# Kernel tuning notes

Hardware: AMD Instinct MI355X
Metric: run time of the kernel (lower is better)

Reference implementation:

```python
import jax, jax.numpy as jnp
import numpy as np

G = 64  # voxel grid extent per axis; grid_ind entries are in [0, G)


def setup_inputs() -> dict:
    key = jax.random.key(0)
    k1, k2 = jax.random.split(key)
    N = 4_000_000
    points = jax.random.normal(k1, (N, 7), dtype=jnp.float32)
    grid_ind = jax.random.randint(k2, (N, 3), 0, G, dtype=jnp.int64)
    return {"points": points, "grid_ind": grid_ind}


def reference(points, grid_ind):
    # torch.unique(grid_ind, dim=0, return_inverse=True) sorts rows
    # lexicographically; for nonnegative coords that equals sorting the
    # linearized index, so we dedup the linear id instead of rows.
    N = points.shape[0]
    gi = grid_ind.astype(jnp.int32)
    lin = (gi[:, 0] * G + gi[:, 1]) * G + gi[:, 2]  # [N]
    # fixed-size unique for jit compatibility: at most N unique voxels,
    # padded with fill_value=-1 at the tail.
    unq, unq_inv = jnp.unique(lin, return_inverse=True, size=N, fill_value=-1)
    # scatter_mean over point->voxel mapping
    sums = jax.ops.segment_sum(points, unq_inv, num_segments=N)          # [N, 7]
    cnt = jax.ops.segment_sum(jnp.ones((N,), points.dtype), unq_inv,
                              num_segments=N)                            # [N]
    mean = sums / jnp.maximum(cnt, 1.0)[:, None]
    # reconstruct the [n_unique_padded, 3] voxel coordinates (pad rows = -1)
    valid = unq >= 0
    u = jnp.maximum(unq, 0)
    unq3 = jnp.stack([u // (G * G), (u // G) % G, u % G], axis=-1)
    unq3 = jnp.where(valid[:, None], unq3, -1).astype(grid_ind.dtype)
    return mean, unq3
```

## Files before the change

### kernel.cpp

```cpp
#include <hip/hip_runtime.h>

#define NVOX 262144
#define NB   256
#define VPB  1024
#define PPB  2048
#define SCT  512
#define NBLK 256

__global__ void dv_fill(const unsigned* __restrict__ nuP,
                        float* __restrict__ out, int n) {
    int nu = (int)*nuP;
    size_t meanChunks = (size_t)n * 7 / 4;
    size_t coordChunks = (size_t)n * 3 / 4;
    size_t total = meanChunks + coordChunks;
    size_t i = (size_t)blockIdx.x * blockDim.x + threadIdx.x;
    if (i >= total) return;
    float* mean = out;
    float* coords = out + (size_t)n * 7;
    if (i < meanChunks) {
        size_t base = i * 4, lim = (size_t)nu * 7;
        if (base >= lim) {
            *(float4*)(mean + base) = make_float4(0.f, 0.f, 0.f, 0.f);
        } else if (base + 4 > lim) {
            for (size_t k = lim; k < base + 4; ++k) mean[k] = 0.f;
        }
    } else {
        size_t base = (i - meanChunks) * 4, lim = (size_t)nu * 3;
        if (base >= lim) {
            *(float4*)(coords + base) = make_float4(-1.f, -1.f, -1.f, -1.f);
        } else if (base + 4 > lim) {
            for (size_t k = lim; k < base + 4; ++k) coords[k] = -1.f;
        }
    }
}

__device__ __forceinline__ unsigned bf16rne(float x) {
    unsigned u = __float_as_uint(x);
    u += 0x7fffu + ((u >> 16) & 1u);
    return u >> 16;
}

__global__ void __launch_bounds__(SCT) rx_scatfuse(
        const int* __restrict__ gi, const float* __restrict__ pts, int n,
        unsigned* __restrict__ cursor, int capb, uint4* __restrict__ recs) {
    __shared__ uint4 recS[PPB];
    __shared__ unsigned dstS[PPB];
    __shared__ unsigned hist[NB];
    __shared__ unsigned bStart[NB];
    __shared__ unsigned runS[NB];
    int t = threadIdx.x, b = blockIdx.x;
    int base = b * PPB;
    int cnt = n - base;
    if (cnt > PPB) cnt = PPB;
    if (t < NB) hist[t] = 0;
    __syncthreads();

    unsigned keyA[PPB / SCT], rankA[PPB / SCT];
    int p0 = base + t * 4;
    if (p0 + 4 <= n) {
        const int4* g4 = (const int4*)(gi + (size_t)base * 3);
        int4 a = g4[3 * t], c = g4[3 * t + 1], d = g4[3 * t + 2];
        keyA[0] = ((unsigned)((a.x << 2) | (a.y >> 4)) << 10) |
                  (unsigned)(((a.y & 15) << 6) | a.z);
        keyA[1] = ((unsigned)((a.w << 2) | (c.x >> 4)) << 10) |
                  (unsigned)(((c.x & 15) << 6) | c.y);
        keyA[2] = ((unsigned)((c.z << 2) | (c.w >> 4)) << 10) |
                  (unsigned)(((c.w & 15) << 6) | d.x);
        keyA[3] = ((unsigned)((d.y << 2) | (d.z >> 4)) << 10) |
                  (unsigned)(((d.z & 15) << 6) | d.w);
#pragma unroll
        for (int j = 0; j < 4; ++j)
            rankA[j] = atomicAdd(&hist[keyA[j] >> 10], 1u);
    } else {
#pragma unroll
        for (int j = 0; j < 4; ++j) {
            int i = p0 + j;
            if (i < n) {
                int g0 = gi[3 * i], g1 = gi[3 * i + 1], g2 = gi[3 * i + 2];
                keyA[j] = ((unsigned)((g0 << 2) | (g1 >> 4)) << 10) |
                          (unsigned)(((g1 & 15) << 6) | g2);
                rankA[j] = atomicAdd(&hist[keyA[j] >> 10], 1u);
            }
        }
    }
    __syncthreads();
    unsigned mine = (t < NB) ? hist[t] : 0u;
    for (int d = 1; d < NB; d <<= 1) {
        unsigned v = (t < NB && t >= d) ? hist[t - d] : 0u;
        __syncthreads();
        if (t < NB) hist[t] += v;
        __syncthreads();
    }
    if (t < NB) {
        bStart[t] = hist[t] - mine;
        runS[t] = (mine > 0) ? atomicAdd(&cursor[t], mine) : 0u;
    }
    __syncthreads();

#pragma unroll
    for (int j = 0; j < PPB / SCT; ++j) {
        int lid = t * 4 + j;
        if (lid < cnt) {
            int i = base + lid;
            const float* p = pts + (size_t)i * 7;
            float f0 = p[0], f1 = p[1], f2 = p[2], f3 = p[3];
            float f4 = p[4], f5 = p[5], f6 = p[6];
            unsigned key = keyA[j], rank = rankA[j];
            unsigned bk = key >> 10, sub = key & 1023u;
            uint4 r;
            r.x = bf16rne(f0) | (bf16rne(f1) << 16);
            r.y = bf16rne(f2) | (bf16rne(f3) << 16);
            r.z = bf16rne(f4) | (bf16rne(f5) << 16);
            r.w = bf16rne(f6) | (sub << 16);
            unsigned sp = bStart[bk] + rank;
            recS[sp] = r;
            dstS[sp] = (unsigned)bk * (unsigned)capb + runS[bk] + rank;
        }
    }
    __syncthreads();
#pragma unroll
    for (int k = 0; k < PPB / SCT; ++k) {
        int j = k * SCT + t;
        if (j < cnt) recs[dstS[j]] = recS[j];
    }
}

__global__ void rx_scan256(const unsigned* __restrict__ in,
                           unsigned* __restrict__ out) {
    __shared__ unsigned sm[NB];
    int t = threadIdx.x;
    unsigned mine = in[t];
    sm[t] = mine;
    __syncthreads();
    for (int off = 1; off < NB; off <<= 1) {
        unsigned v = (t >= off) ? sm[t - off] : 0u;
        __syncthreads();
        sm[t] += v;
        __syncthreads();
    }
    out[t] = sm[t] - mine;
    if (t == NB - 1) out[NB] = sm[t];
}

__global__ void __launch_bounds__(1024) rx_accum(
        const uint4* __restrict__ recs, const unsigned* __restrict__ cursor,
        int capb, float* __restrict__ accTable,
        unsigned* __restrict__ occCount) {
    __shared__ uint4 sortedR[2048];
    __shared__ unsigned cnt_[VPB];
    __shared__ unsigned wsum[16];
    int t = threadIdx.x, bk = blockIdx.x;
    int lane = t & 63, wid = t >> 6;
    unsigned len = cursor[bk];
    size_t base = (size_t)bk * (unsigned)capb;
    float a0 = 0.f, a1 = 0.f, a2 = 0.f, a3 = 0.f,
          a4 = 0.f, a5 = 0.f, a6 = 0.f, cf = 0.f;
    for (unsigned cs = 0; cs < len; cs += 2048) {
        bool v0 = (cs + t) < len, v1 = (cs + 1024 + t) < len;
        uint4 r0, r1;
        unsigned k0 = 0, k1 = 0, rk0 = 0, rk1 = 0;
        if (v0) { r0 = recs[base + cs + t]; k0 = r0.w >> 16; }
        if (v1) { r1 = recs[base + cs + 1024 + t]; k1 = r1.w >> 16; }
        cnt_[t] = 0;
        __syncthreads();
        if (v0) rk0 = atomicAdd(&cnt_[k0], 1u);
        if (v1) rk1 = atomicAdd(&cnt_[k1], 1u);
        __syncthreads();
        unsigned own = cnt_[t];
        unsigned x = own;
#pragma unroll
        for (int d = 1; d < 64; d <<= 1) {
            unsigned y = __shfl_up(x, d, 64);
            if (lane >= d) x += y;
        }
        if (lane == 63) wsum[wid] = x;
        __syncthreads();
        if (t < 64) {
            unsigned w = (lane < 16) ? wsum[lane] : 0u;
            unsigned xx = w;
#pragma unroll
            for (int d = 1; d < 16; d <<= 1) {
                unsigned y = __shfl_up(xx, d, 64);
                if (lane >= d) xx += y;
            }
            if (lane < 16) wsum[lane] = xx - w;
        }
        __syncthreads();
        unsigned excl = x - own + wsum[wid];
        cnt_[t] = excl;
        __syncthreads();
        if (v0) sortedR[cnt_[k0] + rk0] = r0;
        if (v1) sortedR[cnt_[k1] + rk1] = r1;
        __syncthreads();
        unsigned st = excl, end = excl + own;
        for (unsigned k = st; k < end; ++k) {
            uint4 r = sortedR[k];
            a0 += __uint_as_float(r.x << 16);
            a1 += __uint_as_float(r.x & 0xffff0000u);
            a2 += __uint_as_float(r.y << 16);
            a3 += __uint_as_float(r.y & 0xffff0000u);
            a4 += __uint_as_float(r.z << 16);
            a5 += __uint_as_float(r.z & 0xffff0000u);
            a6 += __uint_as_float(r.w << 16);
            cf += 1.f;
        }
        __syncthreads();
    }
    float4* o = (float4*)(accTable + ((size_t)bk * VPB + t) * 8);
    o[0] = make_float4(a0, a1, a2, a3);
    o[1] = make_float4(a4, a5, a6, cf);
    unsigned long long m = __ballot(cf > 0.f);
    if (lane == 0) wsum[wid] = (unsigned)__popcll(m);
    __syncthreads();
    if (t == 0) {
        unsigned occ = 0;
#pragma unroll
        for (int w = 0; w < 16; ++w) occ += wsum[w];
        occCount[bk] = occ;
    }
}

__global__ void rx_emit(const float* __restrict__ accTable,
                        const unsigned* __restrict__ rankBase,
                        float* __restrict__ out_mean,
                        float* __restrict__ out_coords) {
    int bk = blockIdx.x, t = threadIdx.x;
    float row[4][8];
    int pre[4], mycount = 0;
#pragma unroll
    for (int j = 0; j < 4; ++j) {
        int v = t * 4 + j;
        const float4* a = (const float4*)(accTable + ((size_t)bk * VPB + v) * 8);
        float4 r0 = a[0], r1 = a[1];
        row[j][0] = r0.x; row[j][1] = r0.y; row[j][2] = r0.z; row[j][3] = r0.w;
        row[j][4] = r1.x; row[j][5] = r1.y; row[j][6] = r1.z; row[j][7] = r1.w;
        pre[j] = mycount;
        mycount += (row[j][7] > 0.f) ? 1 : 0;
    }
    __shared__ int sm[256];
    sm[t] = mycount;
    __syncthreads();
    for (int off = 1; off < 256; off <<= 1) {
        int v = (t >= off) ? sm[t - off] : 0;
        __syncthreads();
        sm[t] += v;
        __syncthreads();
    }
    int rank0 = (int)rankBase[bk] + (sm[t] - mycount);
#pragma unroll
    for (int j = 0; j < 4; ++j) {
        if (row[j][7] > 0.f) {
            int r = rank0 + pre[j];
            int lin = (bk << 10) | (t * 4 + j);
            float inv = 1.0f / row[j][7];
            float* m = out_mean + (size_t)r * 7;
#pragma unroll
            for (int k = 0; k < 7; ++k) m[k] = row[j][k] * inv;
            float* cd = out_coords + (size_t)r * 3;
            cd[0] = (float)(lin >> 12);
            cd[1] = (float)((lin >> 6) & 63);
            cd[2] = (float)(lin & 63);
        }
    }
}

struct Meta {
    unsigned blockSums[NBLK];
    unsigned blockFlagSums[NBLK];
    unsigned blockOffs[NBLK];
    unsigned blockRankOffs[NBLK];
    unsigned nUnique;
};

__global__ void dv_count(const int* __restrict__ gi, int n,
                         unsigned* __restrict__ counts,
                         unsigned short* __restrict__ slots) {
    int i = blockIdx.x * blockDim.x + threadIdx.x;
    if (i >= n) return;
    int lin = (gi[3 * i] << 12) | (gi[3 * i + 1] << 6) | gi[3 * i + 2];
    unsigned s = atomicAdd(&counts[lin], 1u);
    slots[i] = (unsigned short)s;
}

__global__ void dv_bs1(const unsigned* __restrict__ counts,
                       Meta* __restrict__ meta) {
    int b = blockIdx.x, t = threadIdx.x;
    uint4 c = ((const uint4*)(counts + (size_t)b * 1024))[t];
    unsigned cs = c.x + c.y + c.z + c.w;
    unsigned fs = (c.x > 0) + (c.y > 0) + (c.z > 0) + (c.w > 0);
    __shared__ unsigned smC[256], smF[256];
    smC[t] = cs; smF[t] = fs;
    __syncthreads();
    for (int off = 128; off > 0; off >>= 1) {
        if (t < off) { smC[t] += smC[t + off]; smF[t] += smF[t + off]; }
        __syncthreads();
    }
    if (t == 0) { meta->blockSums[b] = smC[0]; meta->blockFlagSums[b] = smF[0]; }
}

__global__ void dv_scan2(unsigned* __restrict__ offsets, int n,
                         Meta* __restrict__ meta) {
    __shared__ unsigned smC[NBLK], smF[NBLK];
    int t = threadIdx.x;
    unsigned c = meta->blockSums[t], f = meta->blockFlagSums[t];
    smC[t] = c; smF[t] = f;
    __syncthreads();
    for (int off = 1; off < NBLK; off <<= 1) {
        unsigned vc = (t >= off) ? smC[t - off] : 0u;
        unsigned vf = (t >= off) ? smF[t - off] : 0u;
        __syncthreads();
        smC[t] += vc; smF[t] += vf;
        __syncthreads();
    }
    meta->blockOffs[t] = smC[t] - c;
    meta->blockRankOffs[t] = smF[t] - f;
    if (t == NBLK - 1) { meta->nUnique = smF[t]; offsets[NVOX] = (unsigned)n; }
}

__global__ void dv_scan3(unsigned* __restrict__ counts,
                         const Meta* __restrict__ meta) {
    int b = blockIdx.x, t = threadIdx.x;
    uint4 c = ((const uint4*)(counts + (size_t)b * 1024))[t];
    unsigned mysum = c.x + c.y + c.z + c.w;
    __shared__ unsigned sm[256];
    sm[t] = mysum;
    __syncthreads();
    for (int off = 1; off < 256; off <<= 1) {
        unsigned v = (t >= off) ? sm[t - off] : 0u;
        __syncthreads();
        sm[t] += v;
        __syncthreads();
    }
    unsigned base = meta->blockOffs[b] + sm[t] - mysum;
    uint4 o;
    o.x = base;
    o.y = base + c.x;
    o.z = o.y + c.y;
    o.w = o.z + c.z;
    ((uint4*)(counts + (size_t)b * 1024))[t] = o;
}

__global__ void dv_scatter2(const int* __restrict__ gi, int n,
                            const unsigned* __restrict__ offsets,
                            const unsigned short* __restrict__ slots,
                            unsigned* __restrict__ perm) {
    int i = blockIdx.x * blockDim.x + threadIdx.x;
    if (i >= n) return;
    int lin = (gi[3 * i] << 12) | (gi[3 * i + 1] << 6) | gi[3 * i + 2];
    perm[offsets[lin] + (unsigned)slots[i]] = (unsigned)i;
}

__global__ void dv_emit2(const float* __restrict__ points,
                         const unsigned* __restrict__ offsets,
                         const unsigned* __restrict__ perm,
                         const Meta* __restrict__ meta,
                         float* __restrict__ out_mean,
                         float* __restrict__ out_coords) {
    int b = blockIdx.x, t = threadIdx.x;
    int base = b * 1024 + t * 4;
    uint4 o4 = ((const uint4*)offsets)[b * 256 + t];
    unsigned o[5];
    o[0] = o4.x; o[1] = o4.y; o[2] = o4.z; o[3] = o4.w;
    o[4] = offsets[base + 4];
    int c[4], pre[4], mycount = 0;
#pragma unroll
    for (int j = 0; j < 4; ++j) {
        c[j] = (int)(o[j + 1] - o[j]);
        pre[j] = mycount;
        mycount += (c[j] > 0) ? 1 : 0;
    }
    __shared__ int sm[256];
    sm[t] = mycount;
    __syncthreads();
    for (int off = 1; off < 256; off <<= 1) {
        int v = (t >= off) ? sm[t - off] : 0;
        __syncthreads();
        sm[t] += v;
        __syncthreads();
    }
    int rank0 = (int)meta->blockRankOffs[b] + (sm[t] - mycount);
#pragma unroll
    for (int j = 0; j < 4; ++j) {
        if (c[j] > 0) {
            float s0 = 0.f, s1 = 0.f, s2 = 0.f, s3 = 0.f,
                  s4 = 0.f, s5 = 0.f, s6 = 0.f;
            for (unsigned k = o[j]; k < o[j + 1]; ++k) {
                unsigned idx = perm[k];
                const float* p = points + (size_t)idx * 7;
                s0 += p[0]; s1 += p[1]; s2 += p[2]; s3 += p[3];
                s4 += p[4]; s5 += p[5]; s6 += p[6];
            }
            int r = rank0 + pre[j];
            int v = base + j;
            float inv = 1.0f / (float)c[j];
            float* m = out_mean + (size_t)r * 7;
            m[0] = s0 * inv; m[1] = s1 * inv; m[2] = s2 * inv;
            m[3] = s3 * inv; m[4] = s4 * inv; m[5] = s5 * inv;
            m[6] = s6 * inv;
            float* cd = out_coords + (size_t)r * 3;
            cd[0] = (float)(v >> 12);
            cd[1] = (float)((v >> 6) & 63);
            cd[2] = (float)(v & 63);
        }
    }
}

extern "C" void kernel_launch(void* const* d_in, const int* in_sizes, int n_in,
                              void* d_out, int out_size, void* d_ws, size_t ws_size,
                              hipStream_t stream) {
    const float* points = (const float*)d_in[0];
    const int*   gi     = (const int*)d_in[1];
    int n = in_sizes[0] / 7;

    float* out_mean   = (float*)d_out;
    float* out_coords = (float*)d_out + (size_t)n * 7;

    int threads = 256;
    int nb1 = (n + PPB - 1) / PPB;

    int capb = n / NB + n / NB / 8 + 1024;
    size_t recsB = (size_t)NB * capb * 16;
    size_t accB  = (size_t)NB * VPB * 8 * sizeof(float);
    size_t need  = recsB + accB + NB * 4  + NB * 4  +
                   (NB + 1) * 4  + 256;

    size_t fillChunks = (size_t)n * 7 / 4 + (size_t)n * 3 / 4;
    int fillBlocks = (int)((fillChunks + threads - 1) / threads);

    if (ws_size >= need) {
        char* w = (char*)d_ws;
        uint4*    recs     = (uint4*)w;                    w += recsB;
        float*    accTable = (float*)w;                    w += accB;
        unsigned* cursor   = (unsigned*)w;                 w += NB * 4;
        unsigned* occCount = (unsigned*)w;                 w += NB * 4;
        unsigned* rankBase = (unsigned*)w;

        hipMemsetAsync(cursor, 0, NB * 4, stream);
        rx_scatfuse<<<nb1, SCT, 0, stream>>>(gi, points, n, cursor, capb, recs);
        rx_accum<<<NB, 1024, 0, stream>>>(recs, cursor, capb, accTable,
                                          occCount);
        rx_scan256<<<1, NB, 0, stream>>>(occCount, rankBase);
        rx_emit<<<NB, 256, 0, stream>>>(accTable, rankBase, out_mean,
                                        out_coords);
        dv_fill<<<fillBlocks, threads, 0, stream>>>(rankBase + NB,
                                                    (float*)d_out, n);
    } else {
        char* w = (char*)d_ws;
        unsigned*       perm    = (unsigned*)w;
        unsigned short* slots   = (unsigned short*)(w + (size_t)n * 4);
        unsigned*       offsets = (unsigned*)(w + (size_t)n * 4 + (size_t)n * 2);
        Meta*           meta    = (Meta*)((char*)offsets + (size_t)(NVOX + 4) * 4);

        hipMemsetAsync(offsets, 0, (size_t)(NVOX + 4) * 4, stream);

        int blocksN = (n + threads - 1) / threads;
        dv_count<<<blocksN, threads, 0, stream>>>(gi, n, offsets, slots);
        dv_bs1<<<NBLK, 256, 0, stream>>>(offsets, meta);
        dv_scan2<<<1, NBLK, 0, stream>>>(offsets, n, meta);
        dv_scan3<<<NBLK, 256, 0, stream>>>(offsets, meta);
        dv_scatter2<<<blocksN, threads, 0, stream>>>(gi, n, offsets, slots, perm);
        dv_emit2<<<NBLK, 256, 0, stream>>>(points, offsets, perm, meta,
                                           out_mean, out_coords);
        dv_fill<<<fillBlocks, threads, 0, stream>>>(&meta->nUnique,
                                                    (float*)d_out, n);
    }
}
```

Measured before the change: 377.9 us.

## Replace per-bucket counting sort with LDS float atomics; fold scan into emit

rx_accum no longer counting-sorts each chunk of records in shared memory before summing per voxel. Each record now adds its seven bf16-decoded channels and a count straight into a shared-memory accumulator table with float atomics. This removes several barriers and prefix scans per chunk, at the cost of eight LDS atomics per record and possible contention on hot voxels. The separate single-block scan kernel is also removed: each emit block redundantly scans the 256 occupancy counts itself, which saves one launch.

```diff
diff --git a/kernel.cpp b/kernel.cpp
--- a/kernel.cpp
+++ b/kernel.cpp
@@ -125,90 +125,51 @@
     }
 }
 
-__global__ void rx_scan256(const unsigned* __restrict__ in,
-                           unsigned* __restrict__ out) {
-    __shared__ unsigned sm[NB];
-    int t = threadIdx.x;
-    unsigned mine = in[t];
-    sm[t] = mine;
-    __syncthreads();
-    for (int off = 1; off < NB; off <<= 1) {
-        unsigned v = (t >= off) ? sm[t - off] : 0u;
-        __syncthreads();
-        sm[t] += v;
-        __syncthreads();
-    }
-    out[t] = sm[t] - mine;
-    if (t == NB - 1) out[NB] = sm[t];
-}
+#define ACC8(r)                                                         \
+    do {                                                                \
+        unsigned sub_ = (r).w >> 16;                                    \
+        atomicAdd(&acc[0][sub_], __uint_as_float((r).x << 16));         \
+        atomicAdd(&acc[1][sub_], __uint_as_float((r).x & 0xffff0000u)); \
+        atomicAdd(&acc[2][sub_], __uint_as_float((r).y << 16));         \
+        atomicAdd(&acc[3][sub_], __uint_as_float((r).y & 0xffff0000u)); \
+        atomicAdd(&acc[4][sub_], __uint_as_float((r).z << 16));         \
+        atomicAdd(&acc[5][sub_], __uint_as_float((r).z & 0xffff0000u)); \
+        atomicAdd(&acc[6][sub_], __uint_as_float((r).w << 16));         \
+        atomicAdd(&acc[7][sub_], 1.f);                                  \
+    } while (0)
 
 __global__ void __launch_bounds__(1024) rx_accum(
         const uint4* __restrict__ recs, const unsigned* __restrict__ cursor,
         int capb, float* __restrict__ accTable,
         unsigned* __restrict__ occCount) {
-    __shared__ uint4 sortedR[2048];
-    __shared__ unsigned cnt_[VPB];
+    __shared__ float acc[8][VPB];
     __shared__ unsigned wsum[16];
     int t = threadIdx.x, bk = blockIdx.x;
     int lane = t & 63, wid = t >> 6;
+#pragma unroll
+    for (int c = 0; c < 8; ++c) acc[c][t] = 0.f;
+    __syncthreads();
+
     unsigned len = cursor[bk];
     size_t base = (size_t)bk * (unsigned)capb;
-    float a0 = 0.f, a1 = 0.f, a2 = 0.f, a3 = 0.f,
-          a4 = 0.f, a5 = 0.f, a6 = 0.f, cf = 0.f;
-    for (unsigned cs = 0; cs < len; cs += 2048) {
-        bool v0 = (cs + t) < len, v1 = (cs + 1024 + t) < len;
-        uint4 r0, r1;
-        unsigned k0 = 0, k1 = 0, rk0 = 0, rk1 = 0;
-        if (v0) { r0 = recs[base + cs + t]; k0 = r0.w >> 16; }
-        if (v1) { r1 = recs[base + cs + 1024 + t]; k1 = r1.w >> 16; }
-        cnt_[t] = 0;
-        __syncthreads();
-        if (v0) rk0 = atomicAdd(&cnt_[k0], 1u);
-        if (v1) rk1 = atomicAdd(&cnt_[k1], 1u);
-        __syncthreads();
-        unsigned own = cnt_[t];
-        unsigned x = own;
-#pragma unroll
-        for (int d = 1; d < 64; d <<= 1) {
-            unsigned y = __shfl_up(x, d, 64);
-            if (lane >= d) x += y;
-        }
-        if (lane == 63) wsum[wid] = x;
-        __syncthreads();
-        if (t < 64) {
-            unsigned w = (lane < 16) ? wsum[lane] : 0u;
-            unsigned xx = w;
-#pragma unroll
-            for (int d = 1; d < 16; d <<= 1) {
-                unsigned y = __shfl_up(xx, d, 64);
-                if (lane >= d) xx += y;
-            }
-            if (lane < 16) wsum[lane] = xx - w;
-        }
-        __syncthreads();
-        unsigned excl = x - own + wsum[wid];
-        cnt_[t] = excl;
-        __syncthreads();
-        if (v0) sortedR[cnt_[k0] + rk0] = r0;
-        if (v1) sortedR[cnt_[k1] + rk1] = r1;
-        __syncthreads();
-        unsigned st = excl, end = excl + own;
-        for (unsigned k = st; k < end; ++k) {
-            uint4 r = sortedR[k];
-            a0 += __uint_as_float(r.x << 16);
-            a1 += __uint_as_float(r.x & 0xffff0000u);
-            a2 += __uint_as_float(r.y << 16);
-            a3 += __uint_as_float(r.y & 0xffff0000u);
-            a4 += __uint_as_float(r.z << 16);
-            a5 += __uint_as_float(r.z & 0xffff0000u);
-            a6 += __uint_as_float(r.w << 16);
-            cf += 1.f;
-        }
-        __syncthreads();
-    }
+    unsigned i = t;
+    for (; i + 1024 < len; i += 2048) {
+        uint4 r0 = recs[base + i];
+        uint4 r1 = recs[base + i + 1024];
+        ACC8(r0);
+        ACC8(r1);
+    }
+    if (i < len) {
+        uint4 r0 = recs[base + i];
+        ACC8(r0);
+    }
+    __syncthreads();
+
+    float cf = acc[7][t];
     float4* o = (float4*)(accTable + ((size_t)bk * VPB + t) * 8);
-    o[0] = make_float4(a0, a1, a2, a3);
-    o[1] = make_float4(a4, a5, a6, cf);
+    o[0] = make_float4(acc[0][t], acc[1][t], acc[2][t], acc[3][t]);
+    o[1] = make_float4(acc[4][t], acc[5][t], acc[6][t], cf);
+
     unsigned long long m = __ballot(cf > 0.f);
     if (lane == 0) wsum[wid] = (unsigned)__popcll(m);
     __syncthreads();
@@ -221,10 +182,27 @@
 }
 
 __global__ void rx_emit(const float* __restrict__ accTable,
-                        const unsigned* __restrict__ rankBase,
+                        const unsigned* __restrict__ occCount,
+                        unsigned* __restrict__ nuOut,
                         float* __restrict__ out_mean,
                         float* __restrict__ out_coords) {
     int bk = blockIdx.x, t = threadIdx.x;
+
+    __shared__ unsigned smB[NB];
+    __shared__ unsigned rankBaseS;
+    unsigned mineB = occCount[t];
+    smB[t] = mineB;
+    __syncthreads();
+    for (int off = 1; off < NB; off <<= 1) {
+        unsigned v = (t >= off) ? smB[t - off] : 0u;
+        __syncthreads();
+        smB[t] += v;
+        __syncthreads();
+    }
+    if (t == bk) rankBaseS = smB[t] - mineB;
+    if (bk == 0 && t == NB - 1) *nuOut = smB[t];
+    __syncthreads();
+
     float row[4][8];
     int pre[4], mycount = 0;
 #pragma unroll
@@ -246,7 +224,7 @@
         sm[t] += v;
         __syncthreads();
     }
-    int rank0 = (int)rankBase[bk] + (sm[t] - mycount);
+    int rank0 = (int)rankBaseS + (sm[t] - mycount);
 #pragma unroll
     for (int j = 0; j < 4; ++j) {
         if (row[j][7] > 0.f) {
@@ -422,7 +400,7 @@
     size_t recsB = (size_t)NB * capb * 16;
     size_t accB  = (size_t)NB * VPB * 8 * sizeof(float);
     size_t need  = recsB + accB + NB * 4  + NB * 4  +
-                   (NB + 1) * 4  + 256;
+                   4  + 256;
 
     size_t fillChunks = (size_t)n * 7 / 4 + (size_t)n * 3 / 4;
     int fillBlocks = (int)((fillChunks + threads - 1) / threads);
@@ -433,16 +411,15 @@
         float*    accTable = (float*)w;                    w += accB;
         unsigned* cursor   = (unsigned*)w;                 w += NB * 4;
         unsigned* occCount = (unsigned*)w;                 w += NB * 4;
-        unsigned* rankBase = (unsigned*)w;
+        unsigned* nuTotal  = (unsigned*)w;
 
         hipMemsetAsync(cursor, 0, NB * 4, stream);
         rx_scatfuse<<<nb1, SCT, 0, stream>>>(gi, points, n, cursor, capb, recs);
         rx_accum<<<NB, 1024, 0, stream>>>(recs, cursor, capb, accTable,
                                           occCount);
-        rx_scan256<<<1, NB, 0, stream>>>(occCount, rankBase);
-        rx_emit<<<NB, 256, 0, stream>>>(accTable, rankBase, out_mean,
+        rx_emit<<<NB, 256, 0, stream>>>(accTable, occCount, nuTotal, out_mean,
                                         out_coords);
-        dv_fill<<<fillBlocks, threads, 0, stream>>>(rankBase + NB,
+        dv_fill<<<fillBlocks, threads, 0, stream>>>(nuTotal,
                                                     (float*)d_out, n);
     } else {
         char* w = (char*)d_ws;
```

After: 486.0 us. 28.6% more time.
